# Performance work log

Measured on AMD Instinct MI355X. Metric: run time of the kernel, lower is better.

The kernel has to match this reference:

```python
import jax, jax.numpy as jnp
import numpy as np

B, T, IN, H, OUT = 2048, 4096, 1, 8, 1


def setup_inputs() -> dict:
    key = jax.random.key(0)
    ks = jax.random.split(key, 11)
    s_in = 1.0 / np.sqrt(H)  # torch nn.LSTM/Linear init scale (uniform +-1/sqrt(H))
    u = lambda k, shape, s: jax.random.uniform(k, shape, jnp.float32, -s, s)
    return {
        "input_seq": jax.random.normal(ks[0], (B, T, IN), jnp.float32),
        # layer 0 (input_size=IN)
        "W_ih0": u(ks[1], (4 * H, IN), s_in),
        "W_hh0": u(ks[2], (4 * H, H), s_in),
        "b_ih0": u(ks[3], (4 * H,), s_in),
        "b_hh0": u(ks[4], (4 * H,), s_in),
        # layer 1 (input_size=H)
        "W_ih1": u(ks[5], (4 * H, H), s_in),
        "W_hh1": u(ks[6], (4 * H, H), s_in),
        "b_ih1": u(ks[7], (4 * H,), s_in),
        "b_hh1": u(ks[8], (4 * H,), s_in),
        # output projection
        "W_lin": u(ks[9], (OUT, H), s_in),
        "b_lin": u(ks[10], (OUT,), s_in),
    }


def _lstm_layer(x_tbi, W_ih, W_hh, b_ih, b_hh):
    """x_tbi: [T, B, in] -> hidden sequence [T, B, H]. PyTorch gate order i,f,g,o."""
    h_dim = W_hh.shape[1]
    # precompute input contribution for all timesteps (hoisted out of the scan)
    xg = jnp.einsum('tbi,gi->tbg', x_tbi, W_ih) + (b_ih + b_hh)  # [T, B, 4H]
    bsz = x_tbi.shape[1]
    h0 = jnp.zeros((bsz, h_dim), x_tbi.dtype)
    c0 = jnp.zeros((bsz, h_dim), x_tbi.dtype)

    def step(carry, xg_t):
        h, c = carry
        gates = xg_t + h @ W_hh.T  # [B, 4H]
        i, f, g, o = jnp.split(gates, 4, axis=-1)
        i = jax.nn.sigmoid(i)
        f = jax.nn.sigmoid(f)
        g = jnp.tanh(g)
        o = jax.nn.sigmoid(o)
        c = f * c + i * g
        h = o * jnp.tanh(c)
        return (h, c), h

    _, hs = jax.lax.scan(step, (h0, c0), xg)
    return hs  # [T, B, H]


def reference(input_seq, W_ih0, W_hh0, b_ih0, b_hh0,
              W_ih1, W_hh1, b_ih1, b_hh1, W_lin, b_lin):
    x = jnp.transpose(input_seq, (1, 0, 2))  # [T, B, IN] (batch_first -> time-major)
    h1 = _lstm_layer(x, W_ih0, W_hh0, b_ih0, b_hh0)   # [T, B, H]
    h2 = _lstm_layer(h1, W_ih1, W_hh1, b_ih1, b_hh1)  # [T, B, H]
    out = jnp.transpose(h2, (1, 0, 2))                # [B, T, H]
    pred = out @ W_lin.T + b_lin                      # [B, T, OUT]
    return pred
```

## Files before the change

### kernel.cpp

```cpp
#include <hip/hip_runtime.h>


constexpr int Bsz = 2048;
constexpr int Tsz = 4096;

template <int CTRL>
__device__ __forceinline__ float dpp(float v) {
    return __int_as_float(
        __builtin_amdgcn_mov_dpp(__float_as_int(v), CTRL, 0xF, 0xF, true));
}

__device__ __forceinline__ float swz16(float v) {
    return __int_as_float(
        __builtin_amdgcn_ds_swizzle(__float_as_int(v), (16 << 10) | 0x1f));
}

__device__ __forceinline__ float bperm(int addr, float v) {
    return __int_as_float(__builtin_amdgcn_ds_bpermute(addr, __float_as_int(v)));
}

__global__ void __launch_bounds__(256, 2) lstm2_mp2(
    const float* __restrict__ x,
    const float* __restrict__ Wih0,
    const float* __restrict__ Whh0,
    const float* __restrict__ bih0,
    const float* __restrict__ bhh0,
    const float* __restrict__ Wih1,
    const float* __restrict__ Whh1,
    const float* __restrict__ bih1,
    const float* __restrict__ bhh1,
    const float* __restrict__ Wlin,
    const float* __restrict__ blin,
    float* __restrict__ out)
{
    const int tid  = threadIdx.x;
    const int lane = tid & 63;
    const int g    = lane & 3;
    const int j    = (lane >> 2) & 7;
    const int L    = (lane >> 5) & 1;
    const int seq  = blockIdx.x * 4 + (tid >> 6);

    const int jm = j ^ 4;
    const int r  = g * 8 + j;
    const int rm = g * 8 + jm;

    const float NL2E  = -1.4426950408889634f;
    const float N2L2E = -2.8853900817779268f;
    const bool  isG   = (g == 2);
    const float ws    = isG ? N2L2E : NL2E;
    const float sA    = isG ? 2.0f : 1.0f;
    const float oA    = isG ? -1.0f : 0.0f;

    const float* __restrict__ Whh = L ? Whh1 : Whh0;
    const float* __restrict__ bih = L ? bih1 : bih0;
    const float* __restrict__ bhh = L ? bhh1 : bhh0;

    float wn1[4], wm1[4], wn2[4], wm2[4];
#pragma unroll
    for (int i = 0; i < 4; ++i) {
        const int k = j ^ i;
        wn1[i] = Whh[r * 8 + k] * ws;
        wm1[i] = Whh[rm * 8 + k] * ws;
        wn2[i] = L ? Wlin[k] : Wih1[r * 8 + k] * ws;
        wm2[i] = L ? Wlin[k] : Wih1[rm * 8 + k] * ws;
    }
    const float bias = (bih[r] + bhh[r]) * ws;
    const float wx   = L ? 0.0f : Wih0[r] * ws;
    const float b2   = L ? blin[0] : 0.0f;
    const float mL   = L ? 1.0f : 0.0f;
    const float keep = 1.0f - mL;
    const int  xaddr = (lane ^ 32) * 4;

    const float* __restrict__ xp = x + (size_t)seq * Tsz;
    float* __restrict__ op       = out + (size_t)seq * Tsz;
    const bool storeLane = (lane == 32);

    float hn0 = 0.0f, hn1 = 0.0f, hn2 = 0.0f, hn3 = 0.0f;
    float c = 0.0f, h = 0.0f;
    float recvA = 0.0f, recvB = 0.0f;

    auto body = [&](float xt, bool fill, float* storePtr) {
        float am1 = wm1[0] * hn0;
        am1 = fmaf(wm1[1], hn1, am1);
        am1 = fmaf(wm1[2], hn2, am1);
        am1 = fmaf(wm1[3], hn3, am1);
        float am2 = wm2[0] * hn0;
        am2 = fmaf(wm2[1], hn1, am2);
        am2 = fmaf(wm2[2], hn2, am2);
        am2 = fmaf(wm2[3], hn3, am2);
        const float s1 = swz16(am1);
        const float s2 = swz16(am2);

        float an1 = fmaf(wx, xt, bias);
        an1 = fmaf(wn1[0], hn0, an1);
        an1 = fmaf(wn1[1], hn1, an1);
        an1 = fmaf(wn1[2], hn2, an1);
        an1 = fmaf(wn1[3], hn3, an1);
        float an2 = fmaf(wn2[0], hn0, b2);
        an2 = fmaf(wn2[1], hn1, an2);
        an2 = fmaf(wn2[2], hn2, an2);
        an2 = fmaf(wn2[3], hn3, an2);

        const float z = fmaf(mL, recvB, an1 + s1);

        float a = fmaf(sA,
                       __builtin_amdgcn_rcpf(1.0f + __builtin_amdgcn_exp2f(z)),
                       oA);
        const float gi = dpp<0x00>(a);
        const float gf = dpp<0x55>(a);
        const float gG = dpp<0xAA>(a);
        const float go = dpp<0xFF>(a);
        c = fmaf(gf, c, gi * gG);
        const float e  = __builtin_amdgcn_exp2f(c * N2L2E);
        const float th = fmaf(2.0f, __builtin_amdgcn_rcpf(1.0f + e), -1.0f);
        h = go * th;

        if (fill) { h *= keep; c *= keep; }

        const float m7  = dpp<0x141>(h);
        const float m15 = dpp<0x140>(h);
        hn0 = h;
        hn1 = dpp<0x1B>(m7);
        hn2 = dpp<0x141>(m15);
        hn3 = dpp<0x1B>(m15);

        const float d2 = an2 + s2;
        if (storePtr && storeLane) *storePtr = d2;
        recvB = recvA;
        recvA = bperm(xaddr, d2);
    };

    body(xp[0], true, nullptr);
    body(xp[1], true, nullptr);
    body(xp[2], true, nullptr);
    body(xp[3], false, nullptr);

    float xc[4];
#pragma unroll
    for (int u = 0; u < 4; ++u) xc[u] = xp[4 + u];
    for (int ck = 0; ck < Tsz / 4; ++ck) {
        const int base = 4 + 4 * ck;
        float xf[4];
#pragma unroll
        for (int u = 0; u < 4; ++u) {
            int idx = base + 4 + u;
            idx = (idx < Tsz) ? idx : (Tsz - 1);
            xf[u] = xp[idx];
        }
#pragma unroll
        for (int u = 0; u < 4; ++u)
            body(xc[u], false, op + (4 * ck + u));
#pragma unroll
        for (int u = 0; u < 4; ++u) xc[u] = xf[u];
    }
}

extern "C" void kernel_launch(void* const* d_in, const int* in_sizes, int n_in,
                              void* d_out, int out_size, void* d_ws, size_t ws_size,
                              hipStream_t stream) {
    const float* x    = (const float*)d_in[0];
    const float* Wih0 = (const float*)d_in[1];
    const float* Whh0 = (const float*)d_in[2];
    const float* bih0 = (const float*)d_in[3];
    const float* bhh0 = (const float*)d_in[4];
    const float* Wih1 = (const float*)d_in[5];
    const float* Whh1 = (const float*)d_in[6];
    const float* bih1 = (const float*)d_in[7];
    const float* bhh1 = (const float*)d_in[8];
    const float* Wlin = (const float*)d_in[9];
    const float* blin = (const float*)d_in[10];
    float* out = (float*)d_out;

    dim3 grid(Bsz / 4);
    dim3 block(256);
    hipLaunchKernelGGL(lstm2_mp2, grid, block, 0, stream,
                       x, Wih0, Whh0, bih0, bhh0,
                       Wih1, Whh1, bih1, bhh1, Wlin, blin, out);
}
```

Before: 901.3 us.

## Process two sequences per wavefront with packed FP32 math

Each wavefront now carries two independent sequences, packed as float2 pairs, and does the matvec and cell arithmetic with v_pk_fma/v_pk_mul/v_pk_add. This halves the grid (Bsz/8 blocks) and amortises cross-lane DPP/swizzle/bpermute setup, while giving two independent dependency chains to fill the latency-bound recurrence. Transcendentals and lane permutes still run per element, so those costs double per wave. Launch bounds drop to one block per CU, and x is loaded as float4 vectors.

```diff
diff --git a/kernel.cpp b/kernel.cpp
--- a/kernel.cpp
+++ b/kernel.cpp
@@ -4,22 +4,51 @@
 constexpr int Bsz = 2048;
 constexpr int Tsz = 4096;
 
+typedef float v2f __attribute__((ext_vector_type(2)));
+typedef float v4f __attribute__((ext_vector_type(4)));
+
 template <int CTRL>
-__device__ __forceinline__ float dpp(float v) {
+__device__ __forceinline__ float dpp1(float v) {
     return __int_as_float(
         __builtin_amdgcn_mov_dpp(__float_as_int(v), CTRL, 0xF, 0xF, true));
 }
-
-__device__ __forceinline__ float swz16(float v) {
+template <int CTRL>
+__device__ __forceinline__ v2f dpp2(v2f v) {
+    v2f r; r.x = dpp1<CTRL>(v.x); r.y = dpp1<CTRL>(v.y); return r;
+}
+
+__device__ __forceinline__ float swz16f(float v) {
     return __int_as_float(
         __builtin_amdgcn_ds_swizzle(__float_as_int(v), (16 << 10) | 0x1f));
 }
-
-__device__ __forceinline__ float bperm(int addr, float v) {
+__device__ __forceinline__ v2f swz16v(v2f v) {
+    v2f r; r.x = swz16f(v.x); r.y = swz16f(v.y); return r;
+}
+
+__device__ __forceinline__ float bpermf(int addr, float v) {
     return __int_as_float(__builtin_amdgcn_ds_bpermute(addr, __float_as_int(v)));
 }
-
-__global__ void __launch_bounds__(256, 2) lstm2_mp2(
+__device__ __forceinline__ v2f bpermv(int addr, v2f v) {
+    v2f r; r.x = bpermf(addr, v.x); r.y = bpermf(addr, v.y); return r;
+}
+
+__device__ __forceinline__ v2f pk_fma(v2f a, v2f b, v2f c) {
+    v2f d;
+    asm("v_pk_fma_f32 %0, %1, %2, %3" : "=v"(d) : "v"(a), "v"(b), "v"(c));
+    return d;
+}
+__device__ __forceinline__ v2f pk_mul(v2f a, v2f b) {
+    v2f d;
+    asm("v_pk_mul_f32 %0, %1, %2" : "=v"(d) : "v"(a), "v"(b));
+    return d;
+}
+__device__ __forceinline__ v2f pk_add(v2f a, v2f b) {
+    v2f d;
+    asm("v_pk_add_f32 %0, %1, %2" : "=v"(d) : "v"(a), "v"(b));
+    return d;
+}
+
+__global__ void __launch_bounds__(256, 1) lstm2_pk2(
     const float* __restrict__ x,
     const float* __restrict__ Wih0,
     const float* __restrict__ Whh0,
@@ -38,7 +67,8 @@
     const int g    = lane & 3;
     const int j    = (lane >> 2) & 7;
     const int L    = (lane >> 5) & 1;
-    const int seq  = blockIdx.x * 4 + (tid >> 6);
+    const int wid  = blockIdx.x * 4 + (tid >> 6);
+    const int seq0 = wid * 2;
 
     const int jm = j ^ 4;
     const int r  = g * 8 + j;
@@ -48,110 +78,127 @@
     const float N2L2E = -2.8853900817779268f;
     const bool  isG   = (g == 2);
     const float ws    = isG ? N2L2E : NL2E;
-    const float sA    = isG ? 2.0f : 1.0f;
-    const float oA    = isG ? -1.0f : 0.0f;
+    const float sAct  = isG ? 2.0f : 1.0f;
+    const float oAct  = isG ? -1.0f : 0.0f;
 
     const float* __restrict__ Whh = L ? Whh1 : Whh0;
     const float* __restrict__ bih = L ? bih1 : bih0;
     const float* __restrict__ bhh = L ? bhh1 : bhh0;
 
-    float wn1[4], wm1[4], wn2[4], wm2[4];
+    v2f wn1[4], wm1[4], wn2[4], wm2[4];
 #pragma unroll
     for (int i = 0; i < 4; ++i) {
         const int k = j ^ i;
-        wn1[i] = Whh[r * 8 + k] * ws;
-        wm1[i] = Whh[rm * 8 + k] * ws;
-        wn2[i] = L ? Wlin[k] : Wih1[r * 8 + k] * ws;
-        wm2[i] = L ? Wlin[k] : Wih1[rm * 8 + k] * ws;
+        const float a1 = Whh[r * 8 + k] * ws;
+        const float a2 = Whh[rm * 8 + k] * ws;
+        const float a3 = L ? Wlin[k] : Wih1[r * 8 + k] * ws;
+        const float a4 = L ? Wlin[k] : Wih1[rm * 8 + k] * ws;
+        wn1[i] = (v2f){a1, a1};
+        wm1[i] = (v2f){a2, a2};
+        wn2[i] = (v2f){a3, a3};
+        wm2[i] = (v2f){a4, a4};
     }
-    const float bias = (bih[r] + bhh[r]) * ws;
-    const float wx   = L ? 0.0f : Wih0[r] * ws;
-    const float b2   = L ? blin[0] : 0.0f;
-    const float mL   = L ? 1.0f : 0.0f;
-    const float keep = 1.0f - mL;
+    const float biasS = (bih[r] + bhh[r]) * ws;
+    const float wxS   = L ? 0.0f : Wih0[r] * ws;
+    const float b2S   = L ? blin[0] : 0.0f;
+    const float mLS   = L ? 1.0f : 0.0f;
+    const float kpS   = 1.0f - mLS;
+    const v2f biasp = (v2f){biasS, biasS};
+    const v2f wxp   = (v2f){wxS, wxS};
+    const v2f b2p   = (v2f){b2S, b2S};
+    const v2f mLp   = (v2f){mLS, mLS};
+    const v2f keepp = (v2f){kpS, kpS};
+    const v2f n2l2p = (v2f){N2L2E, N2L2E};
     const int  xaddr = (lane ^ 32) * 4;
 
-    const float* __restrict__ xp = x + (size_t)seq * Tsz;
-    float* __restrict__ op       = out + (size_t)seq * Tsz;
-    const bool storeLane = (lane == 32);
-
-    float hn0 = 0.0f, hn1 = 0.0f, hn2 = 0.0f, hn3 = 0.0f;
-    float c = 0.0f, h = 0.0f;
-    float recvA = 0.0f, recvB = 0.0f;
-
-    auto body = [&](float xt, bool fill, float* storePtr) {
-        float am1 = wm1[0] * hn0;
-        am1 = fmaf(wm1[1], hn1, am1);
-        am1 = fmaf(wm1[2], hn2, am1);
-        am1 = fmaf(wm1[3], hn3, am1);
-        float am2 = wm2[0] * hn0;
-        am2 = fmaf(wm2[1], hn1, am2);
-        am2 = fmaf(wm2[2], hn2, am2);
-        am2 = fmaf(wm2[3], hn3, am2);
-        const float s1 = swz16(am1);
-        const float s2 = swz16(am2);
-
-        float an1 = fmaf(wx, xt, bias);
-        an1 = fmaf(wn1[0], hn0, an1);
-        an1 = fmaf(wn1[1], hn1, an1);
-        an1 = fmaf(wn1[2], hn2, an1);
-        an1 = fmaf(wn1[3], hn3, an1);
-        float an2 = fmaf(wn2[0], hn0, b2);
-        an2 = fmaf(wn2[1], hn1, an2);
-        an2 = fmaf(wn2[2], hn2, an2);
-        an2 = fmaf(wn2[3], hn3, an2);
-
-        const float z = fmaf(mL, recvB, an1 + s1);
-
-        float a = fmaf(sA,
-                       __builtin_amdgcn_rcpf(1.0f + __builtin_amdgcn_exp2f(z)),
-                       oA);
-        const float gi = dpp<0x00>(a);
-        const float gf = dpp<0x55>(a);
-        const float gG = dpp<0xAA>(a);
-        const float go = dpp<0xFF>(a);
-        c = fmaf(gf, c, gi * gG);
-        const float e  = __builtin_amdgcn_exp2f(c * N2L2E);
-        const float th = fmaf(2.0f, __builtin_amdgcn_rcpf(1.0f + e), -1.0f);
-        h = go * th;
-
-        if (fill) { h *= keep; c *= keep; }
-
-        const float m7  = dpp<0x141>(h);
-        const float m15 = dpp<0x140>(h);
+    const float* __restrict__ xpA = x + (size_t)seq0 * Tsz;
+    const float* __restrict__ xpB = x + (size_t)(seq0 + 1) * Tsz;
+    const bool storeLane = (lane == 32) || (lane == 33);
+    float* __restrict__ myop = out + (size_t)(seq0 + (lane & 1)) * Tsz;
+
+    v2f hn0 = (v2f){0.f, 0.f}, hn1 = hn0, hn2 = hn0, hn3 = hn0;
+    v2f c = hn0, h = hn0;
+    v2f recvA = hn0, recvB = hn0;
+
+    auto body = [&](v2f xt, bool fill, int sidx) {
+        v2f am1 = pk_mul(wm1[0], hn0);
+        am1 = pk_fma(wm1[1], hn1, am1);
+        am1 = pk_fma(wm1[2], hn2, am1);
+        am1 = pk_fma(wm1[3], hn3, am1);
+        v2f am2 = pk_mul(wm2[0], hn0);
+        am2 = pk_fma(wm2[1], hn1, am2);
+        am2 = pk_fma(wm2[2], hn2, am2);
+        am2 = pk_fma(wm2[3], hn3, am2);
+        const v2f s1 = swz16v(am1);
+        const v2f s2 = swz16v(am2);
+
+        v2f an1 = pk_fma(wxp, xt, biasp);
+        an1 = pk_fma(wn1[0], hn0, an1);
+        an1 = pk_fma(wn1[1], hn1, an1);
+        an1 = pk_fma(wn1[2], hn2, an1);
+        an1 = pk_fma(wn1[3], hn3, an1);
+        v2f an2 = pk_fma(wn2[0], hn0, b2p);
+        an2 = pk_fma(wn2[1], hn1, an2);
+        an2 = pk_fma(wn2[2], hn2, an2);
+        an2 = pk_fma(wn2[3], hn3, an2);
+
+        const v2f z = pk_fma(mLp, recvB, pk_add(an1, s1));
+
+        v2f a;
+        a.x = fmaf(sAct,
+                   __builtin_amdgcn_rcpf(1.0f + __builtin_amdgcn_exp2f(z.x)),
+                   oAct);
+        a.y = fmaf(sAct,
+                   __builtin_amdgcn_rcpf(1.0f + __builtin_amdgcn_exp2f(z.y)),
+                   oAct);
+        const v2f gi = dpp2<0x00>(a);
+        const v2f gf = dpp2<0x55>(a);
+        const v2f gG = dpp2<0xAA>(a);
+        const v2f go = dpp2<0xFF>(a);
+        c = pk_fma(gf, c, pk_mul(gi, gG));
+        const v2f cm = pk_mul(c, n2l2p);
+        v2f th;
+        th.x = fmaf(2.0f,
+                    __builtin_amdgcn_rcpf(1.0f + __builtin_amdgcn_exp2f(cm.x)),
+                    -1.0f);
+        th.y = fmaf(2.0f,
+                    __builtin_amdgcn_rcpf(1.0f + __builtin_amdgcn_exp2f(cm.y)),
+                    -1.0f);
+        h = pk_mul(go, th);
+
+        if (fill) { h = pk_mul(h, keepp); c = pk_mul(c, keepp); }
+
+        const v2f m7  = dpp2<0x141>(h);
+        const v2f m15 = dpp2<0x140>(h);
         hn0 = h;
-        hn1 = dpp<0x1B>(m7);
-        hn2 = dpp<0x141>(m15);
-        hn3 = dpp<0x1B>(m15);
-
-        const float d2 = an2 + s2;
-        if (storePtr && storeLane) *storePtr = d2;
+        hn1 = dpp2<0x1B>(m7);
+        hn2 = dpp2<0x141>(m15);
+        hn3 = dpp2<0x1B>(m15);
+
+        const v2f d2 = pk_add(an2, s2);
+        if (sidx >= 0 && storeLane)
+            myop[sidx] = (lane & 1) ? d2.y : d2.x;
         recvB = recvA;
-        recvA = bperm(xaddr, d2);
+        recvA = bpermv(xaddr, d2);
     };
 
-    body(xp[0], true, nullptr);
-    body(xp[1], true, nullptr);
-    body(xp[2], true, nullptr);
-    body(xp[3], false, nullptr);
-
-    float xc[4];
-#pragma unroll
-    for (int u = 0; u < 4; ++u) xc[u] = xp[4 + u];
+    body((v2f){xpA[0], xpB[0]}, true, -1);
+    body((v2f){xpA[1], xpB[1]}, true, -1);
+    body((v2f){xpA[2], xpB[2]}, true, -1);
+    body((v2f){xpA[3], xpB[3]}, false, -1);
+
+    v4f xcA = *(const v4f*)(xpA + 4);
+    v4f xcB = *(const v4f*)(xpB + 4);
     for (int ck = 0; ck < Tsz / 4; ++ck) {
         const int base = 4 + 4 * ck;
-        float xf[4];
-#pragma unroll
-        for (int u = 0; u < 4; ++u) {
-            int idx = base + 4 + u;
-            idx = (idx < Tsz) ? idx : (Tsz - 1);
-            xf[u] = xp[idx];
-        }
+        int pidx = base + 4;
+        if (pidx > Tsz - 4) pidx = Tsz - 4;
+        const v4f xfA = *(const v4f*)(xpA + pidx);
+        const v4f xfB = *(const v4f*)(xpB + pidx);
 #pragma unroll
         for (int u = 0; u < 4; ++u)
-            body(xc[u], false, op + (4 * ck + u));
-#pragma unroll
-        for (int u = 0; u < 4; ++u) xc[u] = xf[u];
+            body((v2f){xcA[u], xcB[u]}, false, 4 * ck + u);
+        xcA = xfA; xcB = xfB;
     }
 }
 
@@ -171,9 +218,9 @@
     const float* blin = (const float*)d_in[10];
     float* out = (float*)d_out;
 
-    dim3 grid(Bsz / 4);
+    dim3 grid(Bsz / 8);
     dim3 block(256);
-    hipLaunchKernelGGL(lstm2_mp2, grid, block, 0, stream,
+    hipLaunchKernelGGL(lstm2_pk2, grid, block, 0, stream,
                        x, Wih0, Whh0, bih0, bhh0,
                        Wih1, Whh1, bih1, bhh1, Wlin, blin, out);
 }
```

Measured after the change: 1.147 ms. 27.2% more time.
